# Kernel tuning notes

Hardware: AMD Instinct MI355X
Metric: run time of the kernel (lower is better)

The kernel has to match this reference:

```python
import jax, jax.numpy as jnp
import numpy as np

TEMP = 1.0
EPS = 1e-6


def trop_linear(x, w, b, temp=TEMP):
    # x: (..., in), w: (out, in) -> (..., out)
    # y_i = temp * logsumexp_j((w_ij + x_j)/temp) + b_i  (soft tropical / max-plus)
    z = x[..., None, :] + w  # (..., out, in)
    y = temp * jax.nn.logsumexp(z / temp, axis=-1)
    return y + b


def trop_layernorm(x, weight, bias, eps=EPS):
    n = x.shape[-1]
    # torch.median returns the lower of the two middle elements for even n
    med = jnp.sort(x, axis=-1)[..., (n - 1) // 2][..., None]
    q75 = jnp.quantile(x, 0.75, axis=-1, keepdims=True)
    q25 = jnp.quantile(x, 0.25, axis=-1, keepdims=True)
    iqr = jnp.maximum(q75 - q25, eps)
    return (x - med) / iqr * weight + bias


def setup_inputs() -> dict:
    key = jax.random.key(0)
    ks = jax.random.split(key, 8)
    B, D_IN, D_H, D_OUT = 1024, 512, 512, 256
    return {
        "x": jax.random.normal(ks[0], (B, D_IN), dtype=jnp.float32),
        "w1": 0.1 * jax.random.normal(ks[1], (D_H, D_IN), dtype=jnp.float32),
        "b1": jnp.zeros((D_H,), dtype=jnp.float32),
        "ln1_w": jnp.ones((D_H,), dtype=jnp.float32),
        "ln1_b": jnp.zeros((D_H,), dtype=jnp.float32),
        "w2": 0.1 * jax.random.normal(ks[2], (D_H, D_H), dtype=jnp.float32),
        "b2": jnp.zeros((D_H,), dtype=jnp.float32),
        "ln2_w": jnp.ones((D_H,), dtype=jnp.float32),
        "ln2_b": jnp.zeros((D_H,), dtype=jnp.float32),
        "w3": 0.1 * jax.random.normal(ks[3], (D_OUT, D_H), dtype=jnp.float32),
        "b3": jnp.zeros((D_OUT,), dtype=jnp.float32),
    }


def reference(x, w1, b1, ln1_w, ln1_b, w2, b2, ln2_w, ln2_b, w3, b3):
    h = trop_linear(x, w1, b1)
    h = trop_layernorm(h, ln1_w, ln1_b)
    h = jnp.maximum(h, 0.0)  # TropicalActivation('relu', threshold=0)
    h = trop_linear(h, w2, b2)
    h = trop_layernorm(h, ln2_w, ln2_b)
    h = jnp.maximum(h, 0.0)
    return trop_linear(h, w3, b3)
```

## Files before the change

kernel.cpp:

```cpp
#include <hip/hip_runtime.h>
#include <math.h>


typedef float v4f __attribute__((ext_vector_type(4)));

#define ELS_B 528
#define LN64f 4.1588830833596715f

__device__ __forceinline__ int pk4_fp8(float a, float b, float c, float d) {
    int p = __builtin_amdgcn_cvt_pk_fp8_f32(a, b, 0, 0);
    p = __builtin_amdgcn_cvt_pk_fp8_f32(c, d, p, 1);
    return p;
}

__global__ __launch_bounds__(256) void expW_frag(const float* __restrict__ w1,
                                                 const float* __restrict__ w2,
                                                 const float* __restrict__ w3,
                                                 uint8_t* __restrict__ Ef) {
    int u = blockIdx.x * 256 + threadIdx.x;
    int lane = u & 63, t = (u >> 6) & 15, S = u >> 10;
    int r = lane & 15, q = lane >> 4;
    const float* w; int tile;
    if (S < 32)      { w = w1; tile = S; }
    else if (S < 64) { w = w2; tile = S - 32; }
    else             { w = w3; tile = S - 64; }
    const float* src = w + (tile * 16 + r) * 512 + t * 32 + q * 8;
    float4 a = *reinterpret_cast<const float4*>(src);
    float4 b = *reinterpret_cast<const float4*>(src + 4);
    int2 o;
    o.x = pk4_fp8(__expf(a.x), __expf(a.y), __expf(a.z), __expf(a.w));
    o.y = pk4_fp8(__expf(b.x), __expf(b.y), __expf(b.z), __expf(b.w));
    *reinterpret_cast<int2*>(Ef + u * 8) = o;
}

__device__ __forceinline__ void load_areg(const uint8_t* Els, int lane, long* areg) {
    const uint8_t* ap = Els + (lane & 3) * ELS_B + ((lane >> 4) & 3) * 8;
#pragma unroll
    for (int t = 0; t < 16; ++t)
        areg[t] = *reinterpret_cast<const long*>(ap + t * 32);
}

template <int NSUB>
__device__ __forceinline__ void prefetchB(const uint8_t* __restrict__ bp,
                                          int s0, long bb[8][4]) {
#pragma unroll
    for (int p = 0; p < 8; ++p)
#pragma unroll
        for (int s = 0; s < NSUB; ++s)
            bb[p][s] = *reinterpret_cast<const long*>(bp + ((s0 + s) * 16 + p) * 512);
}

template <int NSUB>
__device__ __forceinline__ void gemm_body(const uint8_t* __restrict__ bp,
                                          int s0, const long* areg,
                                          long bb[8][4], v4f* acc) {
#pragma unroll
    for (int s = 0; s < NSUB; ++s) acc[s] = (v4f){0.f, 0.f, 0.f, 0.f};
#pragma unroll
    for (int t = 0; t < 16; ++t) {
        long a = areg[t];
        long bcur[NSUB];
#pragma unroll
        for (int s = 0; s < NSUB; ++s) bcur[s] = bb[t & 7][s];
        if (t < 8) {
#pragma unroll
            for (int s = 0; s < NSUB; ++s)
                bb[t & 7][s] =
                    *reinterpret_cast<const long*>(bp + ((s0 + s) * 16 + t + 8) * 512);
        }
#pragma unroll
        for (int s = 0; s < NSUB; ++s)
            acc[s] = __builtin_amdgcn_mfma_f32_16x16x32_fp8_fp8(a, bcur[s],
                                                                acc[s], 0, 0, 0);
    }
}

__device__ __forceinline__ void ln_row(const float* hbuf,
                                       const float* __restrict__ lw,
                                       const float* __restrict__ lb,
                                       uint8_t* Els, float* crow,
                                       int w, int lane) {
    const float4* lw4 = reinterpret_cast<const float4*>(lw + lane * 8);
    const float4* lb4 = reinterpret_cast<const float4*>(lb + lane * 8);
    float4 wa = lw4[0], wb = lw4[1], ba = lb4[0], bbv = lb4[1];

    float h[8], v[8];
    {
        const float* hp = hbuf + w * 512 + lane * 8;
        float4 a = *reinterpret_cast<const float4*>(hp);
        float4 b = *reinterpret_cast<const float4*>(hp + 4);
        h[0] = a.x; h[1] = a.y; h[2] = a.z; h[3] = a.w;
        h[4] = b.x; h[5] = b.y; h[6] = b.z; h[7] = b.w;
#pragma unroll
        for (int j = 0; j < 8; ++j) v[j] = h[j];
    }
#pragma unroll
    for (int k = 2; k <= 512; k <<= 1) {
#pragma unroll
        for (int jj = 256; jj > 0; jj >>= 1) {
            if (jj >= k) continue;
            if (jj >= 8) {
                int lm = jj >> 3;
#pragma unroll
                for (int j = 0; j < 8; ++j) {
                    float pv = __shfl_xor(v[j], lm);
                    bool up = ((((lane << 3) | j) & k) == 0);
                    bool low = ((lane & lm) == 0);
                    v[j] = (up == low) ? fminf(v[j], pv) : fmaxf(v[j], pv);
                }
            } else {
#pragma unroll
                for (int j = 0; j < 8; ++j) {
                    if (j & jj) continue;
                    int jh = j | jj;
                    bool up = ((((lane << 3) | j) & k) == 0);
                    float a = v[j], c = v[jh];
                    float lo = fminf(a, c), hi = fmaxf(a, c);
                    v[j] = up ? lo : hi;
                    v[jh] = up ? hi : lo;
                }
            }
        }
    }
    float s127 = __shfl(v[7], 15);
    float s128 = __shfl(v[0], 16);
    float med  = __shfl(v[7], 31);
    float s383 = __shfl(v[7], 47);
    float s384 = __shfl(v[0], 48);
    float q25 = s127 + 0.75f * (s128 - s127);
    float q75 = s383 + 0.25f * (s384 - s383);
    float inv = 1.0f / fmaxf(q75 - q25, 1e-6f);

    float y[8], cm = 0.0f;
    {
        float lwv[8] = {wa.x, wa.y, wa.z, wa.w, wb.x, wb.y, wb.z, wb.w};
        float lbv[8] = {ba.x, ba.y, ba.z, ba.w, bbv.x, bbv.y, bbv.z, bbv.w};
#pragma unroll
        for (int j = 0; j < 8; ++j) {
            y[j] = fmaxf((h[j] - med) * inv * lwv[j] + lbv[j], 0.0f);
            cm = fmaxf(cm, y[j]);
        }
    }
#pragma unroll
    for (int s = 32; s > 0; s >>= 1) cm = fmaxf(cm, __shfl_xor(cm, s));
    {
        float e[8];
#pragma unroll
        for (int j = 0; j < 8; ++j) e[j] = 64.0f * __expf(y[j] - cm);
        int2 o;
        o.x = pk4_fp8(e[0], e[1], e[2], e[3]);
        o.y = pk4_fp8(e[4], e[5], e[6], e[7]);
        *reinterpret_cast<int2*>(&Els[w * ELS_B + lane * 8]) = o;
    }
    if (lane == 0) crow[w] = cm;
}

__global__ __launch_bounds__(512, 2) void fused_rows(
    const float* __restrict__ x,
    const float* __restrict__ b1,
    const float* __restrict__ ln1w, const float* __restrict__ ln1b,
    const float* __restrict__ b2,
    const float* __restrict__ ln2w, const float* __restrict__ ln2b,
    const float* __restrict__ b3,
    const uint8_t* __restrict__ Ew,
    float* __restrict__ out)
{
    __shared__ uint8_t Els[4 * ELS_B];
    __shared__ float hbuf[4 * 512];
    __shared__ float crow[4];

    const int tid = threadIdx.x;
    const int lane = tid & 63;
    const int w = tid >> 6;
    const int r = lane & 15, q = lane >> 4;
    const int blk = blockIdx.x;

    const uint8_t* bp1 = Ew + lane * 8;
    const uint8_t* bp2 = bp1 + 262144;
    const uint8_t* bp3 = bp1 + 524288;

    long bb[8][4];
    long areg[16];
    v4f acc[4];

    prefetchB<4>(bp1, w * 4, bb);

    {
        int row = tid >> 7, col = (tid & 127) * 4;
        float4 a = *reinterpret_cast<const float4*>(x + blk * 2048 + row * 512 + col);
        *reinterpret_cast<int*>(&Els[row * ELS_B + col]) =
            pk4_fp8(4.0f * __expf(a.x), 4.0f * __expf(a.y),
                    4.0f * __expf(a.z), 4.0f * __expf(a.w));
    }
    __syncthreads();

    load_areg(Els, lane, areg);
    gemm_body<4>(bp1, w * 4, areg, bb, acc);
    if (q == 0) {
#pragma unroll
        for (int s = 0; s < 4; ++s) {
            int col = (w * 4 + s) * 16 + r;
            float bbv = b1[col];
#pragma unroll
            for (int t = 0; t < 4; ++t)
                hbuf[t * 512 + col] = __logf(acc[s][t]) + bbv;
        }
    }
    prefetchB<4>(bp2, w * 4, bb);
    __syncthreads();
    if (w < 4) ln_row(hbuf, ln1w, ln1b, Els, crow, w, lane);
    __syncthreads();

    load_areg(Els, lane, areg);
    gemm_body<4>(bp2, w * 4, areg, bb, acc);
    if (q == 0) {
#pragma unroll
        for (int s = 0; s < 4; ++s) {
            int col = (w * 4 + s) * 16 + r;
            float bbv = b2[col];
#pragma unroll
            for (int t = 0; t < 4; ++t)
                hbuf[t * 512 + col] = __logf(acc[s][t]) + bbv;
        }
    }
    prefetchB<2>(bp3, w * 2, bb);
    __syncthreads();
    if (w < 4) ln_row(hbuf, ln2w, ln2b, Els, crow, w, lane);
    __syncthreads();

    load_areg(Els, lane, areg);
    gemm_body<2>(bp3, w * 2, areg, bb, acc);
    if (q == 0) {
#pragma unroll
        for (int s = 0; s < 2; ++s) {
            int col = (w * 2 + s) * 16 + r;
            float bbv = b3[col] - LN64f;
#pragma unroll
            for (int t = 0; t < 4; ++t)
                out[(blk * 4 + t) * 256 + col] = __logf(acc[s][t]) + crow[t] + bbv;
        }
    }
}

extern "C" void kernel_launch(void* const* d_in, const int* in_sizes, int n_in,
                              void* d_out, int out_size, void* d_ws, size_t ws_size,
                              hipStream_t stream) {
    const float* x    = (const float*)d_in[0];
    const float* w1   = (const float*)d_in[1];
    const float* b1   = (const float*)d_in[2];
    const float* ln1w = (const float*)d_in[3];
    const float* ln1b = (const float*)d_in[4];
    const float* w2   = (const float*)d_in[5];
    const float* b2   = (const float*)d_in[6];
    const float* ln2w = (const float*)d_in[7];
    const float* ln2b = (const float*)d_in[8];
    const float* w3   = (const float*)d_in[9];
    const float* b3   = (const float*)d_in[10];
    float* out = (float*)d_out;

    uint8_t* Ew = (uint8_t*)d_ws;

    expW_frag<<<320, 256, 0, stream>>>(w1, w2, w3, Ew);
    fused_rows<<<256, 512, 0, stream>>>(x, b1, ln1w, ln1b, b2, ln2w, ln2b,
                                        b3, Ew, out);
}
```

Measured before the change: 94.88 us.

## Process two rows per block and split each row's sort across four waves

Each block now handles two rows instead of four, so the grid doubles to 512 blocks and launch bounds ask for four blocks per SM. The layernorm bitonic sort of each 512-element row is spread across four waves, two elements per lane, with cross-wave merge steps going through shared memory and extra barriers. The GEMM epilogue now spreads the log/bias writes across all quadrant lanes instead of only q==0. The intent is higher occupancy and shorter serial sort work per wave. In exchange, every block reads the full weight fragments again for half as many rows, and the sort needs many more __syncthreads.

```diff
diff --git a/kernel.cpp b/kernel.cpp
--- a/kernel.cpp
+++ b/kernel.cpp
@@ -34,7 +34,7 @@
 }
 
 __device__ __forceinline__ void load_areg(const uint8_t* Els, int lane, long* areg) {
-    const uint8_t* ap = Els + (lane & 3) * ELS_B + ((lane >> 4) & 3) * 8;
+    const uint8_t* ap = Els + (lane & 1) * ELS_B + ((lane >> 4) & 3) * 8;
 #pragma unroll
     for (int t = 0; t < 16; ++t)
         areg[t] = *reinterpret_cast<const long*>(ap + t * 32);
@@ -75,87 +75,95 @@
     }
 }
 
-__device__ __forceinline__ void ln_row(const float* hbuf,
-                                       const float* __restrict__ lw,
-                                       const float* __restrict__ lb,
-                                       uint8_t* Els, float* crow,
-                                       int w, int lane) {
-    const float4* lw4 = reinterpret_cast<const float4*>(lw + lane * 8);
-    const float4* lb4 = reinterpret_cast<const float4*>(lb + lane * 8);
-    float4 wa = lw4[0], wb = lw4[1], ba = lb4[0], bbv = lb4[1];
-
-    float h[8], v[8];
-    {
-        const float* hp = hbuf + w * 512 + lane * 8;
-        float4 a = *reinterpret_cast<const float4*>(hp);
-        float4 b = *reinterpret_cast<const float4*>(hp + 4);
-        h[0] = a.x; h[1] = a.y; h[2] = a.z; h[3] = a.w;
-        h[4] = b.x; h[5] = b.y; h[6] = b.z; h[7] = b.w;
-#pragma unroll
-        for (int j = 0; j < 8; ++j) v[j] = h[j];
-    }
-#pragma unroll
-    for (int k = 2; k <= 512; k <<= 1) {
-#pragma unroll
-        for (int jj = 256; jj > 0; jj >>= 1) {
-            if (jj >= k) continue;
-            if (jj >= 8) {
-                int lm = jj >> 3;
-#pragma unroll
-                for (int j = 0; j < 8; ++j) {
-                    float pv = __shfl_xor(v[j], lm);
-                    bool up = ((((lane << 3) | j) & k) == 0);
-                    bool low = ((lane & lm) == 0);
-                    v[j] = (up == low) ? fminf(v[j], pv) : fmaxf(v[j], pv);
-                }
-            } else {
-#pragma unroll
-                for (int j = 0; j < 8; ++j) {
-                    if (j & jj) continue;
-                    int jh = j | jj;
-                    bool up = ((((lane << 3) | j) & k) == 0);
-                    float a = v[j], c = v[jh];
-                    float lo = fminf(a, c), hi = fmaxf(a, c);
-                    v[j] = up ? lo : hi;
-                    v[jh] = up ? hi : lo;
-                }
-            }
-        }
-    }
-    float s127 = __shfl(v[7], 15);
-    float s128 = __shfl(v[0], 16);
-    float med  = __shfl(v[7], 31);
-    float s383 = __shfl(v[7], 47);
-    float s384 = __shfl(v[0], 48);
+__device__ __forceinline__ void sort_shuf(float& v0, float& v1, int lane,
+                                          int ebase, int k, int jjhi) {
+#pragma clang loop unroll(disable)
+    for (int jj = jjhi; jj >= 2; jj >>= 1) {
+        int lm = jj >> 1;
+        bool keepmin = (((ebase & k) == 0) == ((lane & lm) == 0));
+        float p0 = __shfl_xor(v0, lm);
+        float p1 = __shfl_xor(v1, lm);
+        v0 = keepmin ? fminf(v0, p0) : fmaxf(v0, p0);
+        v1 = keepmin ? fminf(v1, p1) : fmaxf(v1, p1);
+    }
+    bool up = ((ebase & k) == 0);
+    float lo = fminf(v0, v1), hi = fmaxf(v0, v1);
+    v0 = up ? lo : hi;
+    v1 = up ? hi : lo;
+}
+
+__device__ __forceinline__ void ln_row4(float* hb,
+                                        const float* __restrict__ lw,
+                                        const float* __restrict__ lb,
+                                        uint8_t* Els_row, float* crow_row,
+                                        float* cmx_row,
+                                        int W, int lane) {
+    const int e0 = W * 128 + lane * 2;
+    float2 lwv = *reinterpret_cast<const float2*>(lw + e0);
+    float2 lbv = *reinterpret_cast<const float2*>(lb + e0);
+    float2 hv = *reinterpret_cast<const float2*>(hb + e0);
+    float h0 = hv.x, h1 = hv.y, v0 = h0, v1 = h1;
+
+#pragma clang loop unroll(disable)
+    for (int k = 2; k <= 128; k <<= 1)
+        sort_shuf(v0, v1, lane, e0, k, (k >> 1) > 64 ? 64 : (k >> 1));
+
+    __syncthreads();
+    *reinterpret_cast<float2*>(hb + e0) = make_float2(v0, v1);
+    __syncthreads();
+    {
+        bool keepmin = (((e0 & 256) == 0) == ((e0 & 128) == 0));
+        float2 p = *reinterpret_cast<const float2*>(hb + (e0 ^ 128));
+        v0 = keepmin ? fminf(v0, p.x) : fmaxf(v0, p.x);
+        v1 = keepmin ? fminf(v1, p.y) : fmaxf(v1, p.y);
+    }
+    sort_shuf(v0, v1, lane, e0, 256, 64);
+
+    __syncthreads();
+    *reinterpret_cast<float2*>(hb + e0) = make_float2(v0, v1);
+    __syncthreads();
+    {
+        bool keepmin = ((e0 & 256) == 0);
+        float2 p = *reinterpret_cast<const float2*>(hb + (e0 ^ 256));
+        v0 = keepmin ? fminf(v0, p.x) : fmaxf(v0, p.x);
+        v1 = keepmin ? fminf(v1, p.y) : fmaxf(v1, p.y);
+    }
+    __syncthreads();
+    *reinterpret_cast<float2*>(hb + e0) = make_float2(v0, v1);
+    __syncthreads();
+    {
+        bool keepmin = ((e0 & 128) == 0);
+        float2 p = *reinterpret_cast<const float2*>(hb + (e0 ^ 128));
+        v0 = keepmin ? fminf(v0, p.x) : fmaxf(v0, p.x);
+        v1 = keepmin ? fminf(v1, p.y) : fmaxf(v1, p.y);
+    }
+    sort_shuf(v0, v1, lane, e0, 512, 64);
+
+    __syncthreads();
+    *reinterpret_cast<float2*>(hb + e0) = make_float2(v0, v1);
+    __syncthreads();
+    float s127 = hb[127], s128 = hb[128], med = hb[255];
+    float s383 = hb[383], s384 = hb[384];
     float q25 = s127 + 0.75f * (s128 - s127);
     float q75 = s383 + 0.25f * (s384 - s383);
     float inv = 1.0f / fmaxf(q75 - q25, 1e-6f);
 
-    float y[8], cm = 0.0f;
-    {
-        float lwv[8] = {wa.x, wa.y, wa.z, wa.w, wb.x, wb.y, wb.z, wb.w};
-        float lbv[8] = {ba.x, ba.y, ba.z, ba.w, bbv.x, bbv.y, bbv.z, bbv.w};
-#pragma unroll
-        for (int j = 0; j < 8; ++j) {
-            y[j] = fmaxf((h[j] - med) * inv * lwv[j] + lbv[j], 0.0f);
-            cm = fmaxf(cm, y[j]);
-        }
-    }
+    float y0 = fmaxf((h0 - med) * inv * lwv.x + lbv.x, 0.0f);
+    float y1 = fmaxf((h1 - med) * inv * lwv.y + lbv.y, 0.0f);
+    float cm = fmaxf(y0, y1);
 #pragma unroll
     for (int s = 32; s > 0; s >>= 1) cm = fmaxf(cm, __shfl_xor(cm, s));
-    {
-        float e[8];
-#pragma unroll
-        for (int j = 0; j < 8; ++j) e[j] = 64.0f * __expf(y[j] - cm);
-        int2 o;
-        o.x = pk4_fp8(e[0], e[1], e[2], e[3]);
-        o.y = pk4_fp8(e[4], e[5], e[6], e[7]);
-        *reinterpret_cast<int2*>(&Els[w * ELS_B + lane * 8]) = o;
-    }
-    if (lane == 0) crow[w] = cm;
-}
-
-__global__ __launch_bounds__(512, 2) void fused_rows(
+    if (lane == 0) cmx_row[W] = cm;
+    __syncthreads();
+    cm = fmaxf(fmaxf(cmx_row[0], cmx_row[1]), fmaxf(cmx_row[2], cmx_row[3]));
+
+    int p = __builtin_amdgcn_cvt_pk_fp8_f32(64.0f * __expf(y0 - cm),
+                                            64.0f * __expf(y1 - cm), 0, 0);
+    *reinterpret_cast<ushort*>(Els_row + e0) = (ushort)p;
+    if (lane == 0 && W == 0) crow_row[0] = cm;
+}
+
+__global__ __launch_bounds__(512, 4) void fused_rows(
     const float* __restrict__ x,
     const float* __restrict__ b1,
     const float* __restrict__ ln1w, const float* __restrict__ ln1b,
@@ -165,14 +173,16 @@
     const uint8_t* __restrict__ Ew,
     float* __restrict__ out)
 {
-    __shared__ uint8_t Els[4 * ELS_B];
-    __shared__ float hbuf[4 * 512];
-    __shared__ float crow[4];
+    __shared__ uint8_t Els[2 * ELS_B];
+    __shared__ float hbuf[2 * 512];
+    __shared__ float crow[2];
+    __shared__ float cmx[2][4];
 
     const int tid = threadIdx.x;
     const int lane = tid & 63;
     const int w = tid >> 6;
     const int r = lane & 15, q = lane >> 4;
+    const int row = w >> 2, W = w & 3;
     const int blk = blockIdx.x;
 
     const uint8_t* bp1 = Ew + lane * 8;
@@ -185,10 +195,10 @@
 
     prefetchB<4>(bp1, w * 4, bb);
 
-    {
-        int row = tid >> 7, col = (tid & 127) * 4;
-        float4 a = *reinterpret_cast<const float4*>(x + blk * 2048 + row * 512 + col);
-        *reinterpret_cast<int*>(&Els[row * ELS_B + col]) =
+    if (tid < 256) {
+        int rr = tid >> 7, col = (tid & 127) * 4;
+        float4 a = *reinterpret_cast<const float4*>(x + blk * 1024 + rr * 512 + col);
+        *reinterpret_cast<int*>(&Els[rr * ELS_B + col]) =
             pk4_fp8(4.0f * __expf(a.x), 4.0f * __expf(a.y),
                     4.0f * __expf(a.z), 4.0f * __expf(a.w));
     }
@@ -196,49 +206,42 @@
 
     load_areg(Els, lane, areg);
     gemm_body<4>(bp1, w * 4, areg, bb, acc);
-    if (q == 0) {
-#pragma unroll
-        for (int s = 0; s < 4; ++s) {
-            int col = (w * 4 + s) * 16 + r;
-            float bbv = b1[col];
-#pragma unroll
-            for (int t = 0; t < 4; ++t)
-                hbuf[t * 512 + col] = __logf(acc[s][t]) + bbv;
-        }
+    {
+        v4f av = (q == 0) ? acc[0] : (q == 1) ? acc[1] : (q == 2) ? acc[2] : acc[3];
+        int col = (w * 4 + q) * 16 + r;
+        float bbv = b1[col];
+        hbuf[col]       = __logf(av[0]) + bbv;
+        hbuf[512 + col] = __logf(av[1]) + bbv;
     }
     prefetchB<4>(bp2, w * 4, bb);
     __syncthreads();
-    if (w < 4) ln_row(hbuf, ln1w, ln1b, Els, crow, w, lane);
+    ln_row4(hbuf + row * 512, ln1w, ln1b, Els + row * ELS_B,
+            crow + row, cmx[row], W, lane);
     __syncthreads();
 
     load_areg(Els, lane, areg);
     gemm_body<4>(bp2, w * 4, areg, bb, acc);
-    if (q == 0) {
-#pragma unroll
-        for (int s = 0; s < 4; ++s) {
-            int col = (w * 4 + s) * 16 + r;
-            float bbv = b2[col];
-#pragma unroll
-            for (int t = 0; t < 4; ++t)
-                hbuf[t * 512 + col] = __logf(acc[s][t]) + bbv;
-        }
+    {
+        v4f av = (q == 0) ? acc[0] : (q == 1) ? acc[1] : (q == 2) ? acc[2] : acc[3];
+        int col = (w * 4 + q) * 16 + r;
+        float bbv = b2[col];
+        hbuf[col]       = __logf(av[0]) + bbv;
+        hbuf[512 + col] = __logf(av[1]) + bbv;
     }
     prefetchB<2>(bp3, w * 2, bb);
     __syncthreads();
-    if (w < 4) ln_row(hbuf, ln2w, ln2b, Els, crow, w, lane);
+    ln_row4(hbuf + row * 512, ln2w, ln2b, Els + row * ELS_B,
+            crow + row, cmx[row], W, lane);
     __syncthreads();
 
     load_areg(Els, lane, areg);
     gemm_body<2>(bp3, w * 2, areg, bb, acc);
-    if (q == 0) {
-#pragma unroll
-        for (int s = 0; s < 2; ++s) {
-            int col = (w * 2 + s) * 16 + r;
-            float bbv = b3[col] - LN64f;
-#pragma unroll
-            for (int t = 0; t < 4; ++t)
-                out[(blk * 4 + t) * 256 + col] = __logf(acc[s][t]) + crow[t] + bbv;
-        }
+    if (q < 2) {
+        v4f av = (q == 0) ? acc[0] : acc[1];
+        int col = (w * 2 + q) * 16 + r;
+        float bbv = b3[col] - LN64f;
+        out[(blk * 2 + 0) * 256 + col] = __logf(av[0]) + crow[0] + bbv;
+        out[(blk * 2 + 1) * 256 + col] = __logf(av[1]) + crow[1] + bbv;
     }
 }
 
@@ -261,6 +264,6 @@
     uint8_t* Ew = (uint8_t*)d_ws;
 
     expW_frag<<<320, 256, 0, stream>>>(w1, w2, w3, Ew);
-    fused_rows<<<256, 512, 0, stream>>>(x, b1, ln1w, ln1b, b2, ln2w, ln2b,
+    fused_rows<<<512, 512, 0, stream>>>(x, b1, ln1w, ln1b, b2, ln2w, ln2b,
                                         b3, Ew, out);
 }
```

After: 105.1 us. 1.11x slower.
